# Kernel tuning notes

Hardware: AMD Instinct MI355X
Metric: run time of the kernel (lower is better)

The kernel has to match this reference:

```python
import jax, jax.numpy as jnp
import numpy as np

EPS = 1e-5
NUM_GROUPS = 32


def setup_inputs() -> dict:
    key = jax.random.key(0)
    ks = jax.random.split(key, 4)
    b, c, h, w = 8, 512, 32, 32
    x = jax.random.normal(ks[0], (b, c, h, w), dtype=jnp.float32)
    gn_weight = jnp.ones((c,), dtype=jnp.float32)
    gn_bias = jnp.zeros((c,), dtype=jnp.float32)
    qkv_w = jax.random.normal(ks[1], (3 * c, c), dtype=jnp.float32) * (1.0 / np.sqrt(c))
    qkv_b = jnp.zeros((3 * c,), dtype=jnp.float32)
    proj_w = jax.random.normal(ks[2], (c, c), dtype=jnp.float32) * (1.0 / np.sqrt(c))
    proj_b = jnp.zeros((c,), dtype=jnp.float32)
    return {"x": x, "gn_weight": gn_weight, "gn_bias": gn_bias,
            "qkv_w": qkv_w, "qkv_b": qkv_b, "proj_w": proj_w, "proj_b": proj_b}


def _group_norm(x, weight, bias):
    b, c, h, w = x.shape
    xg = x.reshape(b, NUM_GROUPS, c // NUM_GROUPS, h, w)
    mean = xg.mean(axis=(2, 3, 4), keepdims=True)
    var = xg.var(axis=(2, 3, 4), keepdims=True)
    xn = ((xg - mean) * jax.lax.rsqrt(var + EPS)).reshape(b, c, h, w)
    return xn * weight[None, :, None, None] + bias[None, :, None, None]


def reference(x, gn_weight, gn_bias, qkv_w, qkv_b, proj_w, proj_b):
    b, c, h, w = x.shape
    scale = c ** (-0.5)
    xn = _group_norm(x, gn_weight, gn_bias)
    # 1x1 conv == per-pixel matmul over channels
    qkv = jnp.einsum('bchw,oc->bohw', xn, qkv_w) + qkv_b[None, :, None, None]
    q, k, v = jnp.split(qkv.reshape(b, 3 * c, h * w), 3, axis=1)  # each [b, c, N]
    attn = jax.nn.softmax(jnp.einsum('bci,bcj->bij', q, k) * scale, axis=-1)
    out = jnp.einsum('bij,bcj->bci', attn, v).reshape(b, c, h, w)
    proj = jnp.einsum('bchw,oc->bohw', out, proj_w) + proj_b[None, :, None, None]
    return x + proj
```

## Files before the change

### kernel.cpp

```cpp
#include <hip/hip_runtime.h>
#include <cmath>

constexpr int Bsz = 8, Cch = 512, NPIX = 1024;
constexpr int NG = 32, CPG = 16;

typedef __attribute__((ext_vector_type(4))) float f32x4;
typedef __attribute__((ext_vector_type(8))) short s16x8;

#define GLOBAL_AS __attribute__((address_space(1)))
#define LDS_AS __attribute__((address_space(3)))

__device__ inline short f2bf(float f) {
  union { float f; unsigned u; } c = {f};
  unsigned r = (c.u + 0x7fffu + ((c.u >> 16) & 1u)) >> 16;
  return (short)r;
}

__device__ inline float wave_reduce_sum(float v) {
#pragma unroll
  for (int off = 32; off > 0; off >>= 1) v += __shfl_xor(v, off, 64);
  return v;
}
__device__ inline float wave_reduce_max(float v) {
#pragma unroll
  for (int off = 32; off > 0; off >>= 1) v = fmaxf(v, __shfl_xor(v, off, 64));
  return v;
}

__global__ __launch_bounds__(256) void cvt_kernel(const float* __restrict__ in1,
                                                  short* __restrict__ out1, int n1,
                                                  const float* __restrict__ in2,
                                                  short* __restrict__ out2, int n2) {
  const int i = (blockIdx.x * 256 + threadIdx.x) * 4;
  const float* in = in1;
  short* out = out1;
  int j = i;
  if (i >= n1) { in = in2; out = out2; j = i - n1; }
  if (j + 3 < (i >= n1 ? n2 : n1)) {
    float4 v = *(const float4*)(in + j);
    short o[4] = {f2bf(v.x), f2bf(v.y), f2bf(v.z), f2bf(v.w)};
    *(uint2*)(out + j) = *(const uint2*)o;
  }
}

__global__ __launch_bounds__(256) void gn_kernel(
    const float* __restrict__ x, const float* __restrict__ w,
    const float* __restrict__ bb, short* __restrict__ xnt) {
  __shared__ float sm[8];
  const int bg = blockIdx.x, b = bg >> 5, g = bg & 31;
  const float* xp = x + ((size_t)(b * Cch + g * CPG)) * NPIX;
  float s = 0.f, ss = 0.f;
  for (int i = threadIdx.x * 4; i < CPG * NPIX; i += 1024) {
    float4 v = *(const float4*)(xp + i);
    s += v.x + v.y + v.z + v.w;
    ss += v.x * v.x + v.y * v.y + v.z * v.z + v.w * v.w;
  }
  s = wave_reduce_sum(s);
  ss = wave_reduce_sum(ss);
  const int wv = threadIdx.x >> 6;
  if ((threadIdx.x & 63) == 0) { sm[wv] = s; sm[4 + wv] = ss; }
  __syncthreads();
  const float tsum = sm[0] + sm[1] + sm[2] + sm[3];
  const float tsq = sm[4] + sm[5] + sm[6] + sm[7];
  const float inv_n = 1.0f / (CPG * NPIX);
  const float mean = tsum * inv_n;
  const float rstd = rsqrtf(tsq * inv_n - mean * mean + 1e-5f);
  float wc[CPG], bc[CPG];
#pragma unroll
  for (int c = 0; c < CPG; ++c) {
    wc[c] = w[g * CPG + c] * rstd;
    bc[c] = bb[g * CPG + c] - mean * wc[c];
  }
  for (int p = threadIdx.x; p < NPIX; p += 256) {
    short ov[CPG];
#pragma unroll
    for (int c = 0; c < CPG; ++c)
      ov[c] = f2bf(xp[(size_t)c * NPIX + p] * wc[c] + bc[c]);
    short* op = xnt + ((size_t)(b * NPIX + p)) * Cch + g * CPG;
    *(uint4*)op = *(const uint4*)&ov[0];
    *(uint4*)(op + 8) = *(const uint4*)&ov[8];
  }
}

template <int BM, int BN, int EPI>
__global__ __launch_bounds__(256) void mfma_gemm(
    const short* __restrict__ A, const short* __restrict__ B, int K, int lda,
    int ldb, long sA, long sB, const float* __restrict__ bias, float alpha,
    void* __restrict__ Cp, long sC, int ldc, void* __restrict__ C2p, long sC2,
    const float* __restrict__ resid, long sR) {
  constexpr int FM = BM / 32, FN = BN / 32;
  constexpr int NA = BM / 64, NB = BN / 64;
  __shared__ __align__(16) short Asl[2][BM * 32];
  __shared__ __align__(16) short Bsl[2][BN * 32];
  const int t = threadIdx.x;
  const int lane = t & 63, wave = t >> 6;
  const int bz = blockIdx.z;
  const int m0 = blockIdx.y * BM, n0 = blockIdx.x * BN;
  A += sA * bz;
  B += sB * bz;

  const short* ga[NA];
  const short* gb[NB];
  int lofA[NA], lofB[NB];
#pragma unroll
  for (int i = 0; i < NA; ++i) {
    const int s = i * 256 + t;
    ga[i] = A + (size_t)(m0 + ((s >> 6) * 16) + (s & 15)) * lda + ((s >> 4) & 3) * 8;
    lofA[i] = s * 8;
  }
#pragma unroll
  for (int i = 0; i < NB; ++i) {
    const int s = i * 256 + t;
    gb[i] = B + (size_t)(n0 + ((s >> 6) * 16) + (s & 15)) * ldb + ((s >> 4) & 3) * 8;
    lofB[i] = s * 8;
  }

#pragma unroll
  for (int i = 0; i < NA; ++i)
    __builtin_amdgcn_global_load_lds((const GLOBAL_AS void*)ga[i],
                                     (LDS_AS void*)&Asl[0][lofA[i]], 16, 0, 0);
#pragma unroll
  for (int i = 0; i < NB; ++i)
    __builtin_amdgcn_global_load_lds((const GLOBAL_AS void*)gb[i],
                                     (LDS_AS void*)&Bsl[0][lofB[i]], 16, 0, 0);

  f32x4 acc[FM][FN] = {};
  const int wm = wave & 1, wn = wave >> 1;
  int cur = 0;

  for (int k0 = 0; k0 < K; k0 += 32) {
    __syncthreads();
    if (k0 + 32 < K) {
      const int nxt = cur ^ 1;
#pragma unroll
      for (int i = 0; i < NA; ++i)
        __builtin_amdgcn_global_load_lds(
            (const GLOBAL_AS void*)(ga[i] + k0 + 32),
            (LDS_AS void*)&Asl[nxt][lofA[i]], 16, 0, 0);
#pragma unroll
      for (int i = 0; i < NB; ++i)
        __builtin_amdgcn_global_load_lds(
            (const GLOBAL_AS void*)(gb[i] + k0 + 32),
            (LDS_AS void*)&Bsl[nxt][lofB[i]], 16, 0, 0);
    }
    s16x8 af[FM], bf[FN];
#pragma unroll
    for (int i = 0; i < FM; ++i)
      af[i] = *(const s16x8*)(&Asl[cur][(wm * FM + i) * 512 + lane * 8]);
#pragma unroll
    for (int i = 0; i < FN; ++i)
      bf[i] = *(const s16x8*)(&Bsl[cur][(wn * FN + i) * 512 + lane * 8]);
#pragma unroll
    for (int im = 0; im < FM; ++im)
#pragma unroll
      for (int in = 0; in < FN; ++in)
        acc[im][in] = __builtin_amdgcn_mfma_f32_16x16x32_bf16(
            af[im], bf[in], acc[im][in], 0, 0, 0);
    cur ^= 1;
  }

  const int quad = lane >> 4, nn = lane & 15;
#pragma unroll
  for (int im = 0; im < FM; ++im) {
#pragma unroll
    for (int in = 0; in < FN; ++in) {
      const int m = m0 + (wm * FM + im) * 16 + quad * 4;
      const int n = n0 + (wn * FN + in) * 16 + nn;
      if (EPI == 0) {
        if (m0 < 1024) {
          short* Cq = (short*)Cp + sC * bz;
          short o[4];
#pragma unroll
          for (int r = 0; r < 4; ++r) o[r] = f2bf(acc[im][in][r] + bias[m + r]);
          *(uint2*)(Cq + (size_t)n * ldc + m) = *(const uint2*)o;
        } else {
          short* Cv = (short*)C2p + sC2 * bz;
#pragma unroll
          for (int r = 0; r < 4; ++r)
            Cv[(size_t)(m - 1024 + r) * ldc + n] =
                f2bf(acc[im][in][r] + bias[m + r]);
        }
      } else if (EPI == 1) {
        float* Cf = (float*)Cp + sC * bz;
#pragma unroll
        for (int r = 0; r < 4; ++r)
          Cf[(size_t)(m + r) * ldc + n] = acc[im][in][r] * alpha;
      } else if (EPI == 2) {
        short* Cs = (short*)Cp + sC * bz;
#pragma unroll
        for (int r = 0; r < 4; ++r)
          Cs[(size_t)(m + r) * ldc + n] = f2bf(acc[im][in][r]);
      } else {
        float* Cf = (float*)Cp + sC * bz;
        const float* R = resid + sR * bz;
#pragma unroll
        for (int r = 0; r < 4; ++r)
          Cf[(size_t)(m + r) * ldc + n] =
              acc[im][in][r] + bias[m + r] + R[(size_t)(m + r) * ldc + n];
      }
    }
  }
}

__global__ __launch_bounds__(256) void softmax_kernel(const float* __restrict__ S,
                                                      short* __restrict__ P) {
  __shared__ float sm[8];
  const float* p = S + (size_t)blockIdx.x * 1024;
  const int t = threadIdx.x;
  float4 v = ((const float4*)p)[t];
  float mx = fmaxf(fmaxf(v.x, v.y), fmaxf(v.z, v.w));
  mx = wave_reduce_max(mx);
  if ((t & 63) == 0) sm[t >> 6] = mx;
  __syncthreads();
  mx = fmaxf(fmaxf(sm[0], sm[1]), fmaxf(sm[2], sm[3]));
  v.x = __expf(v.x - mx);
  v.y = __expf(v.y - mx);
  v.z = __expf(v.z - mx);
  v.w = __expf(v.w - mx);
  float s = v.x + v.y + v.z + v.w;
  s = wave_reduce_sum(s);
  if ((t & 63) == 0) sm[4 + (t >> 6)] = s;
  __syncthreads();
  const float inv = 1.0f / (sm[4] + sm[5] + sm[6] + sm[7]);
  short o[4] = {f2bf(v.x * inv), f2bf(v.y * inv), f2bf(v.z * inv),
                f2bf(v.w * inv)};
  *(uint2*)(P + (size_t)blockIdx.x * 1024 + t * 4) = *(const uint2*)o;
}

extern "C" void kernel_launch(void* const* d_in, const int* in_sizes, int n_in,
                              void* d_out, int out_size, void* d_ws,
                              size_t ws_size, hipStream_t stream) {
  const float* x = (const float*)d_in[0];
  const float* gnw = (const float*)d_in[1];
  const float* gnb = (const float*)d_in[2];
  const float* qkvw = (const float*)d_in[3];
  const float* qkvb = (const float*)d_in[4];
  const float* projw = (const float*)d_in[5];
  const float* projb = (const float*)d_in[6];
  float* out = (float*)d_out;

  char* ws = (char*)d_ws;
  short* xnt = (short*)ws;
  short* qkt = (short*)(ws + (8ull << 20));
  short* vbuf = (short*)(ws + (24ull << 20));
  float* Sbuf = (float*)(ws + (32ull << 20));
  short* Pbuf = (short*)(ws + (64ull << 20));
  short* Ot = (short*)(ws + (80ull << 20));
  short* wq = (short*)(ws + (88ull << 20));
  short* wp = (short*)(ws + (89ull << 20) + (512ull << 10));

  cvt_kernel<<<1024, 256, 0, stream>>>(qkvw, wq, 1536 * 512, projw, wp,
                                       512 * 512);

  gn_kernel<<<Bsz * NG, 256, 0, stream>>>(x, gnw, gnb, xnt);

  mfma_gemm<128, 128, 0><<<dim3(8, 12, Bsz), 256, 0, stream>>>(
      wq, xnt, 512, 512, 512, 0L, 1024L * 512, qkvb, 1.0f, qkt, 1024L * 1024,
      1024, vbuf, 512L * 1024, nullptr, 0L);

  const float scale = 1.0f / sqrtf(512.0f);
  mfma_gemm<128, 128, 1><<<dim3(8, 8, Bsz), 256, 0, stream>>>(
      qkt, qkt + 512, 512, 1024, 1024, 1024L * 1024, 1024L * 1024, nullptr,
      scale, Sbuf, 1024L * 1024, 1024, nullptr, 0L, nullptr, 0L);

  softmax_kernel<<<Bsz * 1024, 256, 0, stream>>>(Sbuf, Pbuf);

  mfma_gemm<128, 64, 2><<<dim3(8, 8, Bsz), 256, 0, stream>>>(
      Pbuf, vbuf, 1024, 1024, 1024, 1024L * 1024, 512L * 1024, nullptr, 1.0f,
      Ot, 1024L * 512, 512, nullptr, 0L, nullptr, 0L);

  mfma_gemm<64, 128, 3><<<dim3(8, 8, Bsz), 256, 0, stream>>>(
      wp, Ot, 512, 512, 512, 0L, 1024L * 512, projb, 1.0f, out, 512L * 1024,
      1024, nullptr, 0L, x, 512L * 1024);
}
```

Baseline: 206.5 us.

## Triple-buffer GEMM LDS staging with explicit vmcnt waits for deeper prefetch

The MFMA GEMM now keeps three LDS buffers instead of two and prefetches the tile two iterations ahead. Before each compute step it waits only until the current tile's global-to-LDS loads have landed, using a partial vmcnt wait and a raw s_barrier instead of __syncthreads. The aim is to hide more global-load latency behind MFMA work. In exchange it uses more LDS, which can lower occupancy, and it issues wasted dummy loads from offset 0 near the end of the K loop.

```diff
diff --git a/kernel.cpp b/kernel.cpp
--- a/kernel.cpp
+++ b/kernel.cpp
@@ -90,8 +90,9 @@
     const float* __restrict__ resid, long sR) {
   constexpr int FM = BM / 32, FN = BN / 32;
   constexpr int NA = BM / 64, NB = BN / 64;
-  __shared__ __align__(16) short Asl[2][BM * 32];
-  __shared__ __align__(16) short Bsl[2][BN * 32];
+  constexpr int WAIT = 2 * (NA + NB);
+  __shared__ __align__(16) short Asl[3][BM * 32];
+  __shared__ __align__(16) short Bsl[3][BN * 32];
   const int t = threadIdx.x;
   const int lane = t & 63, wave = t >> 6;
   const int bz = blockIdx.z;
@@ -115,48 +116,48 @@
     lofB[i] = s * 8;
   }
 
-#pragma unroll
-  for (int i = 0; i < NA; ++i)
-    __builtin_amdgcn_global_load_lds((const GLOBAL_AS void*)ga[i],
-                                     (LDS_AS void*)&Asl[0][lofA[i]], 16, 0, 0);
-#pragma unroll
-  for (int i = 0; i < NB; ++i)
-    __builtin_amdgcn_global_load_lds((const GLOBAL_AS void*)gb[i],
-                                     (LDS_AS void*)&Bsl[0][lofB[i]], 16, 0, 0);
+  auto stage = [&](int koff, int buf) {
+#pragma unroll
+    for (int i = 0; i < NA; ++i)
+      __builtin_amdgcn_global_load_lds((const GLOBAL_AS void*)(ga[i] + koff),
+                                       (LDS_AS void*)&Asl[buf][lofA[i]], 16, 0, 0);
+#pragma unroll
+    for (int i = 0; i < NB; ++i)
+      __builtin_amdgcn_global_load_lds((const GLOBAL_AS void*)(gb[i] + koff),
+                                       (LDS_AS void*)&Bsl[buf][lofB[i]], 16, 0, 0);
+  };
+
+  stage(0, 0);
+  if (K > 32) stage(32, 1);
 
   f32x4 acc[FM][FN] = {};
   const int wm = wave & 1, wn = wave >> 1;
-  int cur = 0;
+  int cb = 0, pb = 2;
 
   for (int k0 = 0; k0 < K; k0 += 32) {
-    __syncthreads();
-    if (k0 + 32 < K) {
-      const int nxt = cur ^ 1;
-#pragma unroll
-      for (int i = 0; i < NA; ++i)
-        __builtin_amdgcn_global_load_lds(
-            (const GLOBAL_AS void*)(ga[i] + k0 + 32),
-            (LDS_AS void*)&Asl[nxt][lofA[i]], 16, 0, 0);
-#pragma unroll
-      for (int i = 0; i < NB; ++i)
-        __builtin_amdgcn_global_load_lds(
-            (const GLOBAL_AS void*)(gb[i] + k0 + 32),
-            (LDS_AS void*)&Bsl[nxt][lofB[i]], 16, 0, 0);
-    }
+    int kp = k0 + 64;
+    if (kp >= K) kp = 0;
+    stage(kp, pb);
+    asm volatile("s_waitcnt vmcnt(%0)" ::"i"(WAIT) : "memory");
+    asm volatile("s_barrier" ::: "memory");
+
     s16x8 af[FM], bf[FN];
 #pragma unroll
     for (int i = 0; i < FM; ++i)
-      af[i] = *(const s16x8*)(&Asl[cur][(wm * FM + i) * 512 + lane * 8]);
+      af[i] = *(const s16x8*)(&Asl[cb][(wm * FM + i) * 512 + lane * 8]);
 #pragma unroll
     for (int i = 0; i < FN; ++i)
-      bf[i] = *(const s16x8*)(&Bsl[cur][(wn * FN + i) * 512 + lane * 8]);
+      bf[i] = *(const s16x8*)(&Bsl[cb][(wn * FN + i) * 512 + lane * 8]);
 #pragma unroll
     for (int im = 0; im < FM; ++im)
 #pragma unroll
       for (int in = 0; in < FN; ++in)
         acc[im][in] = __builtin_amdgcn_mfma_f32_16x16x32_bf16(
             af[im], bf[in], acc[im][in], 0, 0, 0);
-    cur ^= 1;
+
+    asm volatile("s_waitcnt lgkmcnt(0)\n\ts_barrier" ::: "memory");
+    cb = (cb == 2) ? 0 : cb + 1;
+    pb = (pb == 2) ? 0 : pb + 1;
   }
 
   const int quad = lane >> 4, nn = lane & 15;
```

New measurement: 210.3 us. Within noise of the previous version (+1.8%).
